# Performance work log

Hardware: AMD Instinct MI355X
Metric: run time of the kernel (lower is better)

The kernel has to match this reference:

```python
import jax, jax.numpy as jnp
import numpy as np

EPS = 1e-12  # F.normalize eps


def _normalize(x, axis):
    n = jnp.linalg.norm(x, axis=axis, keepdims=True)
    return x / jnp.maximum(n, EPS)


def _channel_equi_vec_normalize(x):
    # x: [B, C, 3, N]
    x_dir = _normalize(x, axis=2)
    x_norm = jnp.linalg.norm(x, axis=2, keepdims=True)   # [B,C,1,N]
    x_nn = _normalize(x_norm, axis=1)
    return x_dir * x_nn


def _se3_w(W):
    # append last column so each row sums to 1
    return jnp.concatenate([W, 1.0 - W.sum(-1, keepdims=True)], axis=-1)


def _vlin(W, x):
    # W: [O, C], x: [B, C, 3, N] -> [B, O, 3, N]
    return jnp.einsum('oc,bcvn->bovn', W, x)


def _slin(W, b, s):
    # W: [O, C], s: [B, C, N] -> [B, O, N]
    return jnp.einsum('oc,bcn->bon', W, s) + b[None, :, None]


def setup_inputs() -> dict:
    key = jax.random.key(0)
    ks = jax.random.split(key, 12)
    B, C, N = 16, 128, 4096
    scale = 0.05
    return {
        'v_input': jax.random.normal(ks[0], (B, C, 3, N), jnp.float32),
        's_input': jax.random.normal(ks[1], (B, C, N), jnp.float32),
        'weight': jax.random.normal(ks[2], (C, C - 1), jnp.float32) * scale,
        'sv_W': jax.random.normal(ks[3], (C, C), jnp.float32) * scale,
        'sv_b': jax.random.normal(ks[4], (C,), jnp.float32) * scale,
        'cross_weight': jax.random.normal(ks[5], (C, C - 1), jnp.float32) * scale,
        'crossfc_weight': jax.random.normal(ks[6], (C, 2 * C - 1), jnp.float32) * scale,
        'vsdir_weight': jax.random.normal(ks[7], (C, C), jnp.float32) * scale,
        'vs_W': jax.random.normal(ks[8], (C, C), jnp.float32) * scale,
        'vs_b': jax.random.normal(ks[9], (C,), jnp.float32) * scale,
        'ss_W': jax.random.normal(ks[10], (C, C), jnp.float32) * scale,
        'ss_b': jax.random.normal(ks[11], (C,), jnp.float32) * scale,
    }


def reference(v_input, s_input, weight, sv_W, sv_b, cross_weight, crossfc_weight,
              vsdir_weight, vs_W, vs_b, ss_W, ss_b):
    # --- vector output (se3 linear over channels) ---
    v_out = _vlin(_se3_w(weight), v_input)                       # [B,O,3,N]

    # --- scalar -> vector invariant scaling (se3: center, scale, re-add mean) ---
    s2v = _normalize(jnp.einsum('os,bsn->bon', sv_W, s_input) + sv_b[None, :, None], axis=1)
    v_mean = v_out.mean(axis=1, keepdims=True)
    v_out = (v_out - v_mean) * s2v[:, :, None, :] + v_mean

    # --- cross branch (se3) ---
    v_dual = _vlin(_se3_w(cross_weight), v_input)
    d_o = v_dual.mean(axis=1, keepdims=True)
    v_o = v_out.mean(axis=1, keepdims=True)
    v_cross = jnp.cross(_channel_equi_vec_normalize(v_dual - d_o), v_out - v_o, axis=2)
    v_cross = v_cross + v_out
    v_out = _vlin(_se3_w(crossfc_weight), jnp.concatenate([v_cross, v_out], axis=1))

    # --- scalar output ---
    v_sR = v_input - v_input.mean(axis=1, keepdims=True)         # se3 centering
    dual_dir = _normalize(jnp.einsum('oc,bcvn->bovn', vsdir_weight, v_sR), axis=2)
    s_from_v = _normalize((v_sR * dual_dir).sum(axis=2), axis=1)  # [B,C,N]
    s_from_v = _slin(vs_W, vs_b, s_from_v)
    s_from_s = _slin(ss_W, ss_b, s_input)
    s_output = s_from_s + s_from_v

    return (v_out, s_output)
```

## Files before the change

### kernel.cpp

```cpp
#include <hip/hip_runtime.h>
#include <math.h>

typedef __attribute__((ext_vector_type(8))) short short8;
typedef __attribute__((ext_vector_type(4))) float floatx4;

#define EPS 1e-12f

#define WS_AMAIN 0
#define WS_ASCAL 51200
#define WS_AFC   83968
#define WS_AVS   116736
#define WS_VDR_B 266240

__device__ __forceinline__ unsigned short f2bf(float f) {
  union { float f; unsigned u; } v; v.f = f;
  unsigned r = v.u + 0x7FFFu + ((v.u >> 16) & 1u);
  return (unsigned short)(r >> 16);
}
__device__ __forceinline__ float bf2f(unsigned u16) {
  union { unsigned u; float f; } v; v.u = u16 << 16;
  return v.f;
}

__device__ __forceinline__ float block_sum_256(float v, float* red) {
  const int t = threadIdx.x;
  red[t] = v;
  __syncthreads();
  for (int s = 128; s > 0; s >>= 1) {
    if (t < s) red[t] += red[t + s];
    __syncthreads();
  }
  float r = red[0];
  __syncthreads();
  return r;
}

__global__ __launch_bounds__(256) void k_pre(
    const float* __restrict__ weight, const float* __restrict__ sv_W,
    const float* __restrict__ cross_w, const float* __restrict__ crossfc_w,
    const float* __restrict__ vsdir_w, const float* __restrict__ vs_W,
    const float* __restrict__ ss_W, unsigned short* __restrict__ wsu,
    float* __restrict__ vdr) {
  __shared__ float red[256];
  const int o = blockIdx.x;
  const int t = threadIdx.x;

  float s1 = block_sum_256((t < 127) ? weight[o * 127 + t] : 0.f, red);
  if (t < 128)
    wsu[WS_AMAIN + o * 128 + t] = f2bf((t < 127) ? weight[o * 127 + t] : 1.f - s1);

  float s2 = block_sum_256((t < 127) ? cross_w[o * 127 + t] : 0.f, red);
  if (t < 128)
    wsu[WS_AMAIN + (128 + o) * 128 + t] = f2bf((t < 127) ? cross_w[o * 127 + t] : 1.f - s2);

  float s4 = block_sum_256((t < 128) ? vsdir_w[o * 128 + t] : 0.f, red);
  if (t < 128)
    wsu[WS_AMAIN + (256 + o) * 128 + t] = f2bf(vsdir_w[o * 128 + t]);
  if (t == 0) vdr[o] = s4;

  float s3 = block_sum_256((t < 255) ? crossfc_w[o * 255 + t] : 0.f, red);
  wsu[WS_AFC + o * 256 + t] = f2bf((t < 255) ? crossfc_w[o * 255 + t] : 1.f - s3);

  if (t < 128) {
    wsu[WS_ASCAL + o * 128 + t]         = f2bf(sv_W[o * 128 + t]);
    wsu[WS_ASCAL + (128 + o) * 128 + t] = f2bf(ss_W[o * 128 + t]);
    wsu[WS_AVS + o * 128 + t]           = f2bf(vs_W[o * 128 + t]);
  }
  if (o == 0) {
    if (t < 128) wsu[WS_AMAIN + 386 * 128 + t] = f2bf(1.f / 128.f);
    for (int l = t; l < 13 * 128; l += 256) wsu[WS_AMAIN + 387 * 128 + l] = 0;
  }
}

__global__ void k_mean(unsigned short* __restrict__ wsu) {
  const int g = blockIdx.x, c = threadIdx.x;
  float s = 0.f;
  for (int o = 0; o < 128; ++o) s += bf2f(wsu[WS_AMAIN + (g * 128 + o) * 128 + c]);
  wsu[WS_AMAIN + (384 + g) * 128 + c] = f2bf(s * (1.f / 128.f));
}

__global__ __launch_bounds__(512, 2) void k_main(
    const float* __restrict__ v_in, const float* __restrict__ s_in,
    const unsigned short* __restrict__ wsu, const float* __restrict__ vdr,
    const float* __restrict__ sv_b, const float* __restrict__ vs_b,
    const float* __restrict__ ss_b,
    float* __restrict__ v_out, float* __restrict__ s_out) {
  const int t = threadIdx.x;
  const int wave = t >> 6, lane = t & 63;
  const int q = lane >> 4, ln = lane & 15;
  const int cg = wave & 3;
  const int rg = wave >> 2;
  const int b = blockIdx.x >> 6;
  const int n0 = (blockIdx.x & 63) * 64;
  const int mycol = cg * 16 + ln;
  const int rb = rg * 64;
  const int rc = cg * 16 + ln;

  __shared__ __align__(16) unsigned short xB[192 * 136];
  __shared__ __align__(16) unsigned short v2B[192 * 136];
  __shared__ __align__(16) unsigned short sB[64 * 136];
  __shared__ float xred[6][2][64];

  {
    const float* vb = v_in + (size_t)b * (128 * 3 * 4096) + n0;
    for (int l = t; l < 6144; l += 512) {
      const int c = l / 48, r = l % 48;
      const int v = r >> 4, j4 = (r & 15) * 4;
      const float4 f = *(const float4*)(vb + (size_t)(c * 3 + v) * 4096 + j4);
      const int base = (v * 64 + j4) * 136 + c;
      xB[base]       = f2bf(f.x);
      xB[base + 136] = f2bf(f.y);
      xB[base + 272] = f2bf(f.z);
      xB[base + 408] = f2bf(f.w);
    }
    const float* sb = s_in + (size_t)b * (128 * 4096) + n0;
    for (int l = t; l < 2048; l += 512) {
      const int c = l >> 4, j4 = (l & 15) * 4;
      const float4 f = *(const float4*)(sb + (size_t)c * 4096 + j4);
      const int base = j4 * 136 + c;
      sB[base]       = f2bf(f.x);
      sB[base + 136] = f2bf(f.y);
      sB[base + 272] = f2bf(f.z);
      sB[base + 408] = f2bf(f.w);
    }
  }
  __syncthreads();

  floatx4 accS[8];
#pragma unroll
  for (int i = 0; i < 8; ++i) accS[i] = (floatx4){0.f, 0.f, 0.f, 0.f};
#pragma unroll
  for (int k = 0; k < 4; ++k) {
    const short8 bf = *(const short8*)(sB + mycol * 136 + k * 32 + q * 8);
    const unsigned short* ap = wsu + WS_ASCAL + (rb + ln) * 128 + k * 32 + q * 8;
#pragma unroll
    for (int mt = 0; mt < 4; ++mt)
      accS[mt] = __builtin_amdgcn_mfma_f32_16x16x32_bf16(
          *(const short8*)(ap + mt * 2048), bf, accS[mt], 0, 0, 0);
    const unsigned short* ap2 = ap + 128 * 128;
#pragma unroll
    for (int mt = 0; mt < 4; ++mt)
      accS[4 + mt] = __builtin_amdgcn_mfma_f32_16x16x32_bf16(
          *(const short8*)(ap2 + mt * 2048), bf, accS[4 + mt], 0, 0, 0);
  }
  float s2v[4][4], tssb[4][4];
  {
    float nrm = 0.f;
#pragma unroll
    for (int mt = 0; mt < 4; ++mt) {
      const float4 bb = *(const float4*)(sv_b + rb + mt * 16 + q * 4);
      const float* bp = (const float*)&bb;
#pragma unroll
      for (int r = 0; r < 4; ++r) {
        const float tv = accS[mt][r] + bp[r];
        s2v[mt][r] = tv;
        nrm += tv * tv;
      }
    }
    nrm += __shfl_xor(nrm, 16);
    nrm += __shfl_xor(nrm, 32);
    if (lane < 16) xred[0][rg][rc] = nrm;
    __syncthreads();
    const float ntot = xred[0][0][rc] + xred[0][1][rc];
    const float inv = 1.f / fmaxf(sqrtf(ntot), EPS);
#pragma unroll
    for (int mt = 0; mt < 4; ++mt)
#pragma unroll
      for (int r = 0; r < 4; ++r) s2v[mt][r] *= inv;
#pragma unroll
    for (int mt = 0; mt < 4; ++mt) {
      const float4 b1 = *(const float4*)(ss_b + rb + mt * 16 + q * 4);
      const float4 b2 = *(const float4*)(vs_b + rb + mt * 16 + q * 4);
      const float* p1 = (const float*)&b1;
      const float* p2 = (const float*)&b2;
#pragma unroll
      for (int r = 0; r < 4; ++r) tssb[mt][r] = accS[4 + mt][r] + p1[r] + p2[r];
    }
  }

  floatx4 accD[5][3];
#pragma unroll
  for (int i = 0; i < 5; ++i)
#pragma unroll
    for (int v = 0; v < 3; ++v) accD[i][v] = (floatx4){0.f, 0.f, 0.f, 0.f};
#pragma unroll
  for (int k = 0; k < 4; ++k) {
    short8 bfv[3];
#pragma unroll
    for (int v = 0; v < 3; ++v)
      bfv[v] = *(const short8*)(xB + (v * 64 + mycol) * 136 + k * 32 + q * 8);
    const unsigned short* ap = wsu + WS_AMAIN + (256 + rb + ln) * 128 + k * 32 + q * 8;
#pragma unroll
    for (int i = 0; i < 4; ++i) {
      const short8 a = *(const short8*)(ap + i * 2048);
#pragma unroll
      for (int v = 0; v < 3; ++v)
        accD[i][v] = __builtin_amdgcn_mfma_f32_16x16x32_bf16(a, bfv[v], accD[i][v], 0, 0, 0);
    }
    const unsigned short* am = wsu + WS_AMAIN + (384 + ln) * 128 + k * 32 + q * 8;
    const short8 a4 = *(const short8*)am;
#pragma unroll
    for (int v = 0; v < 3; ++v)
      accD[4][v] = __builtin_amdgcn_mfma_f32_16x16x32_bf16(a4, bfv[v], accD[4][v], 0, 0, 0);
  }
  float xm[3], vmn[3], dmn[3];
#pragma unroll
  for (int v = 0; v < 3; ++v) {
    vmn[v] = __shfl(accD[4][v][0], ln);
    dmn[v] = __shfl(accD[4][v][1], ln);
    xm[v]  = __shfl(accD[4][v][2], ln);
  }

  {
    float sfv[4][4];
    float ssum = 0.f;
#pragma unroll
    for (int mt = 0; mt < 4; ++mt) {
      const float4 rs4 = *(const float4*)(vdr + rb + mt * 16 + q * 4);
      const float* rp = (const float*)&rs4;
      uint2 pk[3];
#pragma unroll
      for (int v = 0; v < 3; ++v)
        pk[v] = *(const uint2*)(xB + (v * 64 + mycol) * 136 + rb + mt * 16 + q * 4);
#pragma unroll
      for (int r = 0; r < 4; ++r) {
        float d[3], xr[3];
#pragma unroll
        for (int v = 0; v < 3; ++v) {
          d[v] = accD[mt][v][r] - rp[r] * xm[v];
          const unsigned w = (r < 2) ? pk[v].x : pk[v].y;
          xr[v] = bf2f((w >> ((r & 1) * 16)) & 0xffffu) - xm[v];
        }
        const float n2 = d[0] * d[0] + d[1] * d[1] + d[2] * d[2];
        const float dinv = 1.f / fmaxf(sqrtf(n2), EPS);
        const float sv_ = (xr[0] * d[0] + xr[1] * d[1] + xr[2] * d[2]) * dinv;
        sfv[mt][r] = sv_;
        ssum += sv_ * sv_;
      }
    }
    ssum += __shfl_xor(ssum, 16);
    ssum += __shfl_xor(ssum, 32);
    if (lane < 16) xred[1][rg][rc] = ssum;
    __syncthreads();
    const float stot = xred[1][0][rc] + xred[1][1][rc];
    const float sinv = 1.f / fmaxf(sqrtf(stot), EPS);
#pragma unroll
    for (int mt = 0; mt < 4; ++mt) {
      const unsigned lo = (unsigned)f2bf(sfv[mt][0] * sinv) |
                          ((unsigned)f2bf(sfv[mt][1] * sinv) << 16);
      const unsigned hi = (unsigned)f2bf(sfv[mt][2] * sinv) |
                          ((unsigned)f2bf(sfv[mt][3] * sinv) << 16);
      *(uint2*)(sB + mycol * 136 + rb + mt * 16 + q * 4) = make_uint2(lo, hi);
    }
  }

  floatx4 accV[4][3];
#pragma unroll
  for (int i = 0; i < 4; ++i)
#pragma unroll
    for (int v = 0; v < 3; ++v) accV[i][v] = (floatx4){0.f, 0.f, 0.f, 0.f};
#pragma unroll
  for (int k = 0; k < 4; ++k) {
    short8 bfv[3];
#pragma unroll
    for (int v = 0; v < 3; ++v)
      bfv[v] = *(const short8*)(xB + (v * 64 + mycol) * 136 + k * 32 + q * 8);
    const unsigned short* ap = wsu + WS_AMAIN + (rb + ln) * 128 + k * 32 + q * 8;
#pragma unroll
    for (int mt = 0; mt < 4; ++mt) {
      const short8 a = *(const short8*)(ap + mt * 2048);
#pragma unroll
      for (int v = 0; v < 3; ++v)
        accV[mt][v] = __builtin_amdgcn_mfma_f32_16x16x32_bf16(a, bfv[v], accV[mt][v], 0, 0, 0);
    }
  }
  float v2m[3];
#pragma unroll
  for (int v = 0; v < 3; ++v) {
    float s = 0.f;
#pragma unroll
    for (int mt = 0; mt < 4; ++mt)
#pragma unroll
      for (int r = 0; r < 4; ++r) {
        const float val = (accV[mt][v][r] - vmn[v]) * s2v[mt][r] + vmn[v];
        accV[mt][v][r] = val;
        s += val;
      }
    s += __shfl_xor(s, 16);
    s += __shfl_xor(s, 32);
    if (lane < 16) xred[2 + v][rg][rc] = s;
  }
  __syncthreads();
#pragma unroll
  for (int v = 0; v < 3; ++v)
    v2m[v] = (xred[2 + v][0][rc] + xred[2 + v][1][rc]) * (1.f / 128.f);
#pragma unroll
  for (int mt = 0; mt < 4; ++mt)
#pragma unroll
    for (int v = 0; v < 3; ++v) {
      const unsigned lo = (unsigned)f2bf(accV[mt][v][0]) |
                          ((unsigned)f2bf(accV[mt][v][1]) << 16);
      const unsigned hi = (unsigned)f2bf(accV[mt][v][2]) |
                          ((unsigned)f2bf(accV[mt][v][3]) << 16);
      *(uint2*)(v2B + (v * 64 + mycol) * 136 + rb + mt * 16 + q * 4) = make_uint2(lo, hi);
    }

  floatx4 accW[4][3];
#pragma unroll
  for (int i = 0; i < 4; ++i)
#pragma unroll
    for (int v = 0; v < 3; ++v) accW[i][v] = (floatx4){0.f, 0.f, 0.f, 0.f};
#pragma unroll
  for (int k = 0; k < 4; ++k) {
    short8 bfv[3];
#pragma unroll
    for (int v = 0; v < 3; ++v)
      bfv[v] = *(const short8*)(xB + (v * 64 + mycol) * 136 + k * 32 + q * 8);
    const unsigned short* ap = wsu + WS_AMAIN + (128 + rb + ln) * 128 + k * 32 + q * 8;
#pragma unroll
    for (int mt = 0; mt < 4; ++mt) {
      const short8 a = *(const short8*)(ap + mt * 2048);
#pragma unroll
      for (int v = 0; v < 3; ++v)
        accW[mt][v] = __builtin_amdgcn_mfma_f32_16x16x32_bf16(a, bfv[v], accW[mt][v], 0, 0, 0);
    }
  }
  float an[4][4];
  float csum = 0.f;
#pragma unroll
  for (int mt = 0; mt < 4; ++mt)
#pragma unroll
    for (int r = 0; r < 4; ++r) {
      const float a0 = accW[mt][0][r] - dmn[0];
      const float a1 = accW[mt][1][r] - dmn[1];
      const float a2 = accW[mt][2][r] - dmn[2];
      accW[mt][0][r] = a0; accW[mt][1][r] = a1; accW[mt][2][r] = a2;
      const float n2 = a0 * a0 + a1 * a1 + a2 * a2;
      an[mt][r] = sqrtf(n2);
      csum += n2;
    }
  csum += __shfl_xor(csum, 16);
  csum += __shfl_xor(csum, 32);
  if (lane < 16) xred[5][rg][rc] = csum;
  __syncthreads();
  const float ctot = xred[5][0][rc] + xred[5][1][rc];
  const float cninv = 1.f / fmaxf(sqrtf(ctot), EPS);
#pragma unroll
  for (int mt = 0; mt < 4; ++mt) {
    float crv[3][4];
#pragma unroll
    for (int r = 0; r < 4; ++r) {
      const float sc = an[mt][r] / fmaxf(an[mt][r], EPS) * cninv;
      const float h0 = accW[mt][0][r] * sc;
      const float h1 = accW[mt][1][r] * sc;
      const float h2 = accW[mt][2][r] * sc;
      const float w0 = accV[mt][0][r], w1 = accV[mt][1][r], w2 = accV[mt][2][r];
      const float g0 = w0 - v2m[0], g1 = w1 - v2m[1], g2 = w2 - v2m[2];
      crv[0][r] = h1 * g2 - h2 * g1 + w0;
      crv[1][r] = h2 * g0 - h0 * g2 + w1;
      crv[2][r] = h0 * g1 - h1 * g0 + w2;
    }
#pragma unroll
    for (int v = 0; v < 3; ++v) {
      const unsigned lo = (unsigned)f2bf(crv[v][0]) | ((unsigned)f2bf(crv[v][1]) << 16);
      const unsigned hi = (unsigned)f2bf(crv[v][2]) | ((unsigned)f2bf(crv[v][3]) << 16);
      *(uint2*)(xB + (v * 64 + mycol) * 136 + rb + mt * 16 + q * 4) = make_uint2(lo, hi);
    }
  }
  __syncthreads();

  floatx4 accO[4][3];
  floatx4 accP[4];
#pragma unroll
  for (int i = 0; i < 4; ++i) {
    accP[i] = (floatx4){0.f, 0.f, 0.f, 0.f};
#pragma unroll
    for (int v = 0; v < 3; ++v) accO[i][v] = (floatx4){0.f, 0.f, 0.f, 0.f};
  }
#pragma unroll
  for (int ks = 0; ks < 8; ++ks) {
    const unsigned short* src = (ks < 4) ? xB : v2B;
    const int kk = ks & 3;
    short8 bfv[3];
#pragma unroll
    for (int v = 0; v < 3; ++v)
      bfv[v] = *(const short8*)(src + (v * 64 + mycol) * 136 + kk * 32 + q * 8);
    const unsigned short* afc = wsu + WS_AFC + (rb + ln) * 256 + ks * 32 + q * 8;
#pragma unroll
    for (int mt = 0; mt < 4; ++mt) {
      const short8 a = *(const short8*)(afc + mt * 4096);
#pragma unroll
      for (int v = 0; v < 3; ++v)
        accO[mt][v] = __builtin_amdgcn_mfma_f32_16x16x32_bf16(a, bfv[v], accO[mt][v], 0, 0, 0);
    }
    if (ks < 4) {
      const short8 bfs = *(const short8*)(sB + mycol * 136 + kk * 32 + q * 8);
      const unsigned short* avs = wsu + WS_AVS + (rb + ln) * 128 + kk * 32 + q * 8;
#pragma unroll
      for (int mt = 0; mt < 4; ++mt)
        accP[mt] = __builtin_amdgcn_mfma_f32_16x16x32_bf16(
            *(const short8*)(avs + mt * 2048), bfs, accP[mt], 0, 0, 0);
    }
  }

  const int gc = n0 + mycol;
  float* vob = v_out + (size_t)b * (128 * 3 * 4096) + gc;
  float* sob = s_out + (size_t)b * (128 * 4096) + gc;
#pragma unroll
  for (int mt = 0; mt < 4; ++mt)
#pragma unroll
    for (int r = 0; r < 4; ++r) {
      const int o = rb + mt * 16 + q * 4 + r;
#pragma unroll
      for (int v = 0; v < 3; ++v)
        vob[(size_t)(o * 3 + v) * 4096] = accO[mt][v][r];
      sob[(size_t)o * 4096] = accP[mt][r] + tssb[mt][r];
    }
}

extern "C" void kernel_launch(void* const* d_in, const int* in_sizes, int n_in,
                              void* d_out, int out_size, void* d_ws, size_t ws_size,
                              hipStream_t stream) {
  const float* v_in      = (const float*)d_in[0];
  const float* s_in      = (const float*)d_in[1];
  const float* weight    = (const float*)d_in[2];
  const float* sv_W      = (const float*)d_in[3];
  const float* sv_b      = (const float*)d_in[4];
  const float* cross_w   = (const float*)d_in[5];
  const float* crossfc_w = (const float*)d_in[6];
  const float* vsdir_w   = (const float*)d_in[7];
  const float* vs_W      = (const float*)d_in[8];
  const float* vs_b      = (const float*)d_in[9];
  const float* ss_W      = (const float*)d_in[10];
  const float* ss_b      = (const float*)d_in[11];

  float* out = (float*)d_out;
  float* v_out = out;
  float* s_out = out + (size_t)16 * 128 * 3 * 4096;
  unsigned short* wsu = (unsigned short*)d_ws;
  float* vdr = (float*)((char*)d_ws + WS_VDR_B);

  hipLaunchKernelGGL(k_pre, dim3(128), dim3(256), 0, stream,
                     weight, sv_W, cross_w, crossfc_w, vsdir_w, vs_W, ss_W, wsu, vdr);
  hipLaunchKernelGGL(k_mean, dim3(2), dim3(128), 0, stream, wsu);
  hipLaunchKernelGGL(k_main, dim3(1024), dim3(512), 0, stream,
                     v_in, s_in, wsu, vdr, sv_b, vs_b, ss_b, v_out, s_out);
}
```

Baseline: 410.1 us.

## Halve column tile, split rows over four wave groups, compute channel means in-kernel

Each block now covers 32 columns instead of 64, and its 8 waves are split into 4 row groups of 32 output channels and 2 column groups. This cuts LDS and per-thread accumulators so launch bounds can allow 4 blocks per CU, and doubles the grid. The k_mean kernel is removed: the v_out and v_dual channel means are now reduced in-kernel from the MFMA accumulators through shared memory, costing two extra block barriers. The workspace rows that held the precomputed means are zeroed instead. Weight fragments are reloaded by twice as many blocks.

Result: faster. 393.6 us (-4.0%).

```diff
diff --git a/kernel.cpp b/kernel.cpp
--- a/kernel.cpp
+++ b/kernel.cpp
@@ -67,19 +67,12 @@
     wsu[WS_AVS + o * 128 + t]           = f2bf(vs_W[o * 128 + t]);
   }
   if (o == 0) {
+    for (int l = t; l < 16 * 128; l += 256) wsu[WS_AMAIN + 384 * 128 + l] = 0;
     if (t < 128) wsu[WS_AMAIN + 386 * 128 + t] = f2bf(1.f / 128.f);
-    for (int l = t; l < 13 * 128; l += 256) wsu[WS_AMAIN + 387 * 128 + l] = 0;
-  }
-}
-
-__global__ void k_mean(unsigned short* __restrict__ wsu) {
-  const int g = blockIdx.x, c = threadIdx.x;
-  float s = 0.f;
-  for (int o = 0; o < 128; ++o) s += bf2f(wsu[WS_AMAIN + (g * 128 + o) * 128 + c]);
-  wsu[WS_AMAIN + (384 + g) * 128 + c] = f2bf(s * (1.f / 128.f));
-}
-
-__global__ __launch_bounds__(512, 2) void k_main(
+  }
+}
+
+__global__ __launch_bounds__(512, 4) void k_main(
     const float* __restrict__ v_in, const float* __restrict__ s_in,
     const unsigned short* __restrict__ wsu, const float* __restrict__ vdr,
     const float* __restrict__ sv_b, const float* __restrict__ vs_b,
@@ -88,34 +81,33 @@
   const int t = threadIdx.x;
   const int wave = t >> 6, lane = t & 63;
   const int q = lane >> 4, ln = lane & 15;
-  const int cg = wave & 3;
-  const int rg = wave >> 2;
-  const int b = blockIdx.x >> 6;
-  const int n0 = (blockIdx.x & 63) * 64;
+  const int cg = wave & 1;
+  const int rg = wave >> 1;
+  const int b = blockIdx.x >> 7;
+  const int n0 = (blockIdx.x & 127) * 32;
   const int mycol = cg * 16 + ln;
-  const int rb = rg * 64;
-  const int rc = cg * 16 + ln;
-
-  __shared__ __align__(16) unsigned short xB[192 * 136];
-  __shared__ __align__(16) unsigned short v2B[192 * 136];
-  __shared__ __align__(16) unsigned short sB[64 * 136];
-  __shared__ float xred[6][2][64];
+  const int rb = rg * 32;
+
+  __shared__ __align__(16) unsigned short xB[96 * 136];
+  __shared__ __align__(16) unsigned short v2B[96 * 136];
+  __shared__ __align__(16) unsigned short sB[32 * 136];
+  __shared__ float xred[8][4][32];
 
   {
     const float* vb = v_in + (size_t)b * (128 * 3 * 4096) + n0;
-    for (int l = t; l < 6144; l += 512) {
-      const int c = l / 48, r = l % 48;
-      const int v = r >> 4, j4 = (r & 15) * 4;
+    for (int l = t; l < 3072; l += 512) {
+      const int c = l / 24, r = l % 24;
+      const int v = r >> 3, j4 = (r & 7) * 4;
       const float4 f = *(const float4*)(vb + (size_t)(c * 3 + v) * 4096 + j4);
-      const int base = (v * 64 + j4) * 136 + c;
+      const int base = (v * 32 + j4) * 136 + c;
       xB[base]       = f2bf(f.x);
       xB[base + 136] = f2bf(f.y);
       xB[base + 272] = f2bf(f.z);
       xB[base + 408] = f2bf(f.w);
     }
     const float* sb = s_in + (size_t)b * (128 * 4096) + n0;
-    for (int l = t; l < 2048; l += 512) {
-      const int c = l >> 4, j4 = (l & 15) * 4;
+    for (int l = t; l < 1024; l += 512) {
+      const int c = l >> 3, j4 = (l & 7) * 4;
       const float4 f = *(const float4*)(sb + (size_t)c * 4096 + j4);
       const int base = j4 * 136 + c;
       sB[base]       = f2bf(f.x);
@@ -126,28 +118,28 @@
   }
   __syncthreads();
 
-  floatx4 accS[8];
-#pragma unroll
-  for (int i = 0; i < 8; ++i) accS[i] = (floatx4){0.f, 0.f, 0.f, 0.f};
+  floatx4 accS[4];
+#pragma unroll
+  for (int i = 0; i < 4; ++i) accS[i] = (floatx4){0.f, 0.f, 0.f, 0.f};
 #pragma unroll
   for (int k = 0; k < 4; ++k) {
     const short8 bf = *(const short8*)(sB + mycol * 136 + k * 32 + q * 8);
     const unsigned short* ap = wsu + WS_ASCAL + (rb + ln) * 128 + k * 32 + q * 8;
 #pragma unroll
-    for (int mt = 0; mt < 4; ++mt)
+    for (int mt = 0; mt < 2; ++mt)
       accS[mt] = __builtin_amdgcn_mfma_f32_16x16x32_bf16(
           *(const short8*)(ap + mt * 2048), bf, accS[mt], 0, 0, 0);
     const unsigned short* ap2 = ap + 128 * 128;
 #pragma unroll
-    for (int mt = 0; mt < 4; ++mt)
-      accS[4 + mt] = __builtin_amdgcn_mfma_f32_16x16x32_bf16(
-          *(const short8*)(ap2 + mt * 2048), bf, accS[4 + mt], 0, 0, 0);
-  }
-  float s2v[4][4], tssb[4][4];
+    for (int mt = 0; mt < 2; ++mt)
+      accS[2 + mt] = __builtin_amdgcn_mfma_f32_16x16x32_bf16(
+          *(const short8*)(ap2 + mt * 2048), bf, accS[2 + mt], 0, 0, 0);
+  }
+  float s2v[2][4], tssb[2][4];
   {
     float nrm = 0.f;
 #pragma unroll
-    for (int mt = 0; mt < 4; ++mt) {
+    for (int mt = 0; mt < 2; ++mt) {
       const float4 bb = *(const float4*)(sv_b + rb + mt * 16 + q * 4);
       const float* bp = (const float*)&bb;
 #pragma unroll
@@ -159,28 +151,29 @@
     }
     nrm += __shfl_xor(nrm, 16);
     nrm += __shfl_xor(nrm, 32);
-    if (lane < 16) xred[0][rg][rc] = nrm;
+    if (lane < 16) xred[0][rg][mycol] = nrm;
     __syncthreads();
-    const float ntot = xred[0][0][rc] + xred[0][1][rc];
+    const float ntot = xred[0][0][mycol] + xred[0][1][mycol] +
+                       xred[0][2][mycol] + xred[0][3][mycol];
     const float inv = 1.f / fmaxf(sqrtf(ntot), EPS);
 #pragma unroll
-    for (int mt = 0; mt < 4; ++mt)
+    for (int mt = 0; mt < 2; ++mt)
 #pragma unroll
       for (int r = 0; r < 4; ++r) s2v[mt][r] *= inv;
 #pragma unroll
-    for (int mt = 0; mt < 4; ++mt) {
+    for (int mt = 0; mt < 2; ++mt) {
       const float4 b1 = *(const float4*)(ss_b + rb + mt * 16 + q * 4);
       const float4 b2 = *(const float4*)(vs_b + rb + mt * 16 + q * 4);
       const float* p1 = (const float*)&b1;
       const float* p2 = (const float*)&b2;
 #pragma unroll
-      for (int r = 0; r < 4; ++r) tssb[mt][r] = accS[4 + mt][r] + p1[r] + p2[r];
-    }
-  }
-
-  floatx4 accD[5][3];
-#pragma unroll
-  for (int i = 0; i < 5; ++i)
+      for (int r = 0; r < 4; ++r) tssb[mt][r] = accS[2 + mt][r] + p1[r] + p2[r];
+    }
+  }
+
+  floatx4 accD[3][3];
+#pragma unroll
+  for (int i = 0; i < 3; ++i)
 #pragma unroll
     for (int v = 0; v < 3; ++v) accD[i][v] = (floatx4){0.f, 0.f, 0.f, 0.f};
 #pragma unroll
@@ -188,10 +181,10 @@
     short8 bfv[3];
 #pragma unroll
     for (int v = 0; v < 3; ++v)
-      bfv[v] = *(const short8*)(xB + (v * 64 + mycol) * 136 + k * 32 + q * 8);
+      bfv[v] = *(const short8*)(xB + (v * 32 + mycol) * 136 + k * 32 + q * 8);
     const unsigned short* ap = wsu + WS_AMAIN + (256 + rb + ln) * 128 + k * 32 + q * 8;
 #pragma unroll
-    for (int i = 0; i < 4; ++i) {
+    for (int i = 0; i < 2; ++i) {
       const short8 a = *(const short8*)(ap + i * 2048);
 #pragma unroll
       for (int v = 0; v < 3; ++v)
@@ -201,27 +194,23 @@
     const short8 a4 = *(const short8*)am;
 #pragma unroll
     for (int v = 0; v < 3; ++v)
-      accD[4][v] = __builtin_amdgcn_mfma_f32_16x16x32_bf16(a4, bfv[v], accD[4][v], 0, 0, 0);
-  }
-  float xm[3], vmn[3], dmn[3];
-#pragma unroll
-  for (int v = 0; v < 3; ++v) {
-    vmn[v] = __shfl(accD[4][v][0], ln);
-    dmn[v] = __shfl(accD[4][v][1], ln);
-    xm[v]  = __shfl(accD[4][v][2], ln);
-  }
+      accD[2][v] = __builtin_amdgcn_mfma_f32_16x16x32_bf16(a4, bfv[v], accD[2][v], 0, 0, 0);
+  }
+  float xm[3];
+#pragma unroll
+  for (int v = 0; v < 3; ++v) xm[v] = __shfl(accD[2][v][2], ln);
 
   {
-    float sfv[4][4];
+    float sfv[2][4];
     float ssum = 0.f;
 #pragma unroll
-    for (int mt = 0; mt < 4; ++mt) {
+    for (int mt = 0; mt < 2; ++mt) {
       const float4 rs4 = *(const float4*)(vdr + rb + mt * 16 + q * 4);
       const float* rp = (const float*)&rs4;
       uint2 pk[3];
 #pragma unroll
       for (int v = 0; v < 3; ++v)
-        pk[v] = *(const uint2*)(xB + (v * 64 + mycol) * 136 + rb + mt * 16 + q * 4);
+        pk[v] = *(const uint2*)(xB + (v * 32 + mycol) * 136 + rb + mt * 16 + q * 4);
 #pragma unroll
       for (int r = 0; r < 4; ++r) {
         float d[3], xr[3];
@@ -240,12 +229,13 @@
     }
     ssum += __shfl_xor(ssum, 16);
     ssum += __shfl_xor(ssum, 32);
-    if (lane < 16) xred[1][rg][rc] = ssum;
+    if (lane < 16) xred[1][rg][mycol] = ssum;
     __syncthreads();
-    const float stot = xred[1][0][rc] + xred[1][1][rc];
+    const float stot = xred[1][0][mycol] + xred[1][1][mycol] +
+                       xred[1][2][mycol] + xred[1][3][mycol];
     const float sinv = 1.f / fmaxf(sqrtf(stot), EPS);
 #pragma unroll
-    for (int mt = 0; mt < 4; ++mt) {
+    for (int mt = 0; mt < 2; ++mt) {
       const unsigned lo = (unsigned)f2bf(sfv[mt][0] * sinv) |
                           ((unsigned)f2bf(sfv[mt][1] * sinv) << 16);
       const unsigned hi = (unsigned)f2bf(sfv[mt][2] * sinv) |
@@ -254,9 +244,9 @@
     }
   }
 
-  floatx4 accV[4][3];
-#pragma unroll
-  for (int i = 0; i < 4; ++i)
+  floatx4 accV[2][3];
+#pragma unroll
+  for (int i = 0; i < 2; ++i)
 #pragma unroll
     for (int v = 0; v < 3; ++v) accV[i][v] = (floatx4){0.f, 0.f, 0.f, 0.f};
 #pragma unroll
@@ -264,22 +254,38 @@
     short8 bfv[3];
 #pragma unroll
     for (int v = 0; v < 3; ++v)
-      bfv[v] = *(const short8*)(xB + (v * 64 + mycol) * 136 + k * 32 + q * 8);
+      bfv[v] = *(const short8*)(xB + (v * 32 + mycol) * 136 + k * 32 + q * 8);
     const unsigned short* ap = wsu + WS_AMAIN + (rb + ln) * 128 + k * 32 + q * 8;
 #pragma unroll
-    for (int mt = 0; mt < 4; ++mt) {
+    for (int mt = 0; mt < 2; ++mt) {
       const short8 a = *(const short8*)(ap + mt * 2048);
 #pragma unroll
       for (int v = 0; v < 3; ++v)
         accV[mt][v] = __builtin_amdgcn_mfma_f32_16x16x32_bf16(a, bfv[v], accV[mt][v], 0, 0, 0);
     }
   }
-  float v2m[3];
 #pragma unroll
   for (int v = 0; v < 3; ++v) {
     float s = 0.f;
 #pragma unroll
-    for (int mt = 0; mt < 4; ++mt)
+    for (int mt = 0; mt < 2; ++mt)
+#pragma unroll
+      for (int r = 0; r < 4; ++r) s += accV[mt][v][r];
+    s += __shfl_xor(s, 16);
+    s += __shfl_xor(s, 32);
+    if (lane < 16) xred[2 + v][rg][mycol] = s;
+  }
+  __syncthreads();
+  float vmn[3], v2m[3];
+#pragma unroll
+  for (int v = 0; v < 3; ++v)
+    vmn[v] = (xred[2 + v][0][mycol] + xred[2 + v][1][mycol] +
+              xred[2 + v][2][mycol] + xred[2 + v][3][mycol]) * (1.f / 128.f);
+#pragma unroll
+  for (int v = 0; v < 3; ++v) {
+    float s = 0.f;
+#pragma unroll
+    for (int mt = 0; mt < 2; ++mt)
 #pragma unroll
       for (int r = 0; r < 4; ++r) {
         const float val = (accV[mt][v][r] - vmn[v]) * s2v[mt][r] + vmn[v];
@@ -288,26 +294,27 @@
       }
     s += __shfl_xor(s, 16);
     s += __shfl_xor(s, 32);
-    if (lane < 16) xred[2 + v][rg][rc] = s;
+    if (lane < 16) xred[5 + v][rg][mycol] = s;
   }
   __syncthreads();
 #pragma unroll
   for (int v = 0; v < 3; ++v)
-    v2m[v] = (xred[2 + v][0][rc] + xred[2 + v][1][rc]) * (1.f / 128.f);
-#pragma unroll
-  for (int mt = 0; mt < 4; ++mt)
+    v2m[v] = (xred[5 + v][0][mycol] + xred[5 + v][1][mycol] +
+              xred[5 + v][2][mycol] + xred[5 + v][3][mycol]) * (1.f / 128.f);
+#pragma unroll
+  for (int mt = 0; mt < 2; ++mt)
 #pragma unroll
     for (int v = 0; v < 3; ++v) {
       const unsigned lo = (unsigned)f2bf(accV[mt][v][0]) |
                           ((unsigned)f2bf(accV[mt][v][1]) << 16);
       const unsigned hi = (unsigned)f2bf(accV[mt][v][2]) |
                           ((unsigned)f2bf(accV[mt][v][3]) << 16);
-      *(uint2*)(v2B + (v * 64 + mycol) * 136 + rb + mt * 16 + q * 4) = make_uint2(lo, hi);
-    }
-
-  floatx4 accW[4][3];
-#pragma unroll
-  for (int i = 0; i < 4; ++i)
+      *(uint2*)(v2B + (v * 32 + mycol) * 136 + rb + mt * 16 + q * 4) = make_uint2(lo, hi);
+    }
+
+  floatx4 accW[2][3];
+#pragma unroll
+  for (int i = 0; i < 2; ++i)
 #pragma unroll
     for (int v = 0; v < 3; ++v) accW[i][v] = (floatx4){0.f, 0.f, 0.f, 0.f};
 #pragma unroll
@@ -315,20 +322,37 @@
     short8 bfv[3];
 #pragma unroll
     for (int v = 0; v < 3; ++v)
-      bfv[v] = *(const short8*)(xB + (v * 64 + mycol) * 136 + k * 32 + q * 8);
+      bfv[v] = *(const short8*)(xB + (v * 32 + mycol) * 136 + k * 32 + q * 8);
     const unsigned short* ap = wsu + WS_AMAIN + (128 + rb + ln) * 128 + k * 32 + q * 8;
 #pragma unroll
-    for (int mt = 0; mt < 4; ++mt) {
+    for (int mt = 0; mt < 2; ++mt) {
       const short8 a = *(const short8*)(ap + mt * 2048);
 #pragma unroll
       for (int v = 0; v < 3; ++v)
         accW[mt][v] = __builtin_amdgcn_mfma_f32_16x16x32_bf16(a, bfv[v], accW[mt][v], 0, 0, 0);
     }
   }
-  float an[4][4];
+#pragma unroll
+  for (int v = 0; v < 3; ++v) {
+    float s = 0.f;
+#pragma unroll
+    for (int mt = 0; mt < 2; ++mt)
+#pragma unroll
+      for (int r = 0; r < 4; ++r) s += accW[mt][v][r];
+    s += __shfl_xor(s, 16);
+    s += __shfl_xor(s, 32);
+    if (lane < 16) xred[2 + v][rg][mycol] = s;
+  }
+  __syncthreads();
+  float dmn[3];
+#pragma unroll
+  for (int v = 0; v < 3; ++v)
+    dmn[v] = (xred[2 + v][0][mycol] + xred[2 + v][1][mycol] +
+              xred[2 + v][2][mycol] + xred[2 + v][3][mycol]) * (1.f / 128.f);
+  float an[2][4];
   float csum = 0.f;
 #pragma unroll
-  for (int mt = 0; mt < 4; ++mt)
+  for (int mt = 0; mt < 2; ++mt)
 #pragma unroll
     for (int r = 0; r < 4; ++r) {
       const float a0 = accW[mt][0][r] - dmn[0];
@@ -341,12 +365,13 @@
     }
   csum += __shfl_xor(csum, 16);
   csum += __shfl_xor(csum, 32);
-  if (lane < 16) xred[5][rg][rc] = csum;
-  __syncthreads();
-  const float ctot = xred[5][0][rc] + xred[5][1][rc];
+  if (lane < 16) xred[0][rg][mycol] = csum;
+  __syncthreads();
+  const float ctot = xred[0][0][mycol] + xred[0][1][mycol] +
+                     xred[0][2][mycol] + xred[0][3][mycol];
   const float cninv = 1.f / fmaxf(sqrtf(ctot), EPS);
 #pragma unroll
-  for (int mt = 0; mt < 4; ++mt) {
+  for (int mt = 0; mt < 2; ++mt) {
     float crv[3][4];
 #pragma unroll
     for (int r = 0; r < 4; ++r) {
@@ -364,15 +389,15 @@
     for (int v = 0; v < 3; ++v) {
       const unsigned lo = (unsigned)f2bf(crv[v][0]) | ((unsigned)f2bf(crv[v][1]) << 16);
       const unsigned hi = (unsigned)f2bf(crv[v][2]) | ((unsigned)f2bf(crv[v][3]) << 16);
-      *(uint2*)(xB + (v * 64 + mycol) * 136 + rb + mt * 16 + q * 4) = make_uint2(lo, hi);
-    }
-  }
-  __syncthreads();
-
-  floatx4 accO[4][3];
-  floatx4 accP[4];
-#pragma unroll
-  for (int i = 0; i < 4; ++i) {
+      *(uint2*)(xB + (v * 32 + mycol) * 136 + rb + mt * 16 + q * 4) = make_uint2(lo, hi);
+    }
+  }
+  __syncthreads();
+
+  floatx4 accO[2][3];
+  floatx4 accP[2];
+#pragma unroll
+  for (int i = 0; i < 2; ++i) {
     accP[i] = (floatx4){0.f, 0.f, 0.f, 0.f};
 #pragma unroll
     for (int v = 0; v < 3; ++v) accO[i][v] = (floatx4){0.f, 0.f, 0.f, 0.f};
@@ -384,10 +409,10 @@
     short8 bfv[3];
 #pragma unroll
     for (int v = 0; v < 3; ++v)
-      bfv[v] = *(const short8*)(src + (v * 64 + mycol) * 136 + kk * 32 + q * 8);
+      bfv[v] = *(const short8*)(src + (v * 32 + mycol) * 136 + kk * 32 + q * 8);
     const unsigned short* afc = wsu + WS_AFC + (rb + ln) * 256 + ks * 32 + q * 8;
 #pragma unroll
-    for (int mt = 0; mt < 4; ++mt) {
+    for (int mt = 0; mt < 2; ++mt) {
       const short8 a = *(const short8*)(afc + mt * 4096);
 #pragma unroll
       for (int v = 0; v < 3; ++v)
@@ -397,7 +422,7 @@
       const short8 bfs = *(const short8*)(sB + mycol * 136 + kk * 32 + q * 8);
       const unsigned short* avs = wsu + WS_AVS + (rb + ln) * 128 + kk * 32 + q * 8;
 #pragma unroll
-      for (int mt = 0; mt < 4; ++mt)
+      for (int mt = 0; mt < 2; ++mt)
         accP[mt] = __builtin_amdgcn_mfma_f32_16x16x32_bf16(
             *(const short8*)(avs + mt * 2048), bfs, accP[mt], 0, 0, 0);
     }
@@ -407,7 +432,7 @@
   float* vob = v_out + (size_t)b * (128 * 3 * 4096) + gc;
   float* sob = s_out + (size_t)b * (128 * 4096) + gc;
 #pragma unroll
-  for (int mt = 0; mt < 4; ++mt)
+  for (int mt = 0; mt < 2; ++mt)
 #pragma unroll
     for (int r = 0; r < 4; ++r) {
       const int o = rb + mt * 16 + q * 4 + r;
@@ -442,7 +467,6 @@
 
   hipLaunchKernelGGL(k_pre, dim3(128), dim3(256), 0, stream,
                      weight, sv_W, cross_w, crossfc_w, vsdir_w, vs_W, ss_W, wsu, vdr);
-  hipLaunchKernelGGL(k_mean, dim3(2), dim3(128), 0, stream, wsu);
-  hipLaunchKernelGGL(k_main, dim3(1024), dim3(512), 0, stream,
+  hipLaunchKernelGGL(k_main, dim3(2048), dim3(512), 0, stream,
                      v_in, s_in, wsu, vdr, sv_b, vs_b, ss_b, v_out, s_out);
 }
```
